# Optimization experiments

Measured on AMD Instinct MI355X. Metric: run time of the kernel, lower is better.

Reference implementation:

```python
import jax, jax.numpy as jnp
import numpy as np

B, T, C, H = 16, 4096, 256, 256

def setup_inputs() -> dict:
    key = jax.random.key(0)
    kx, kwi, kbi, kwh, kbh = jax.random.split(key, 5)
    s = 1.0 / np.sqrt(C)
    return {
        "x": jax.random.normal(kx, (B, T, C), dtype=jnp.float32),
        "Wi": jax.random.uniform(kwi, (H, C), dtype=jnp.float32, minval=-s, maxval=s),
        "bi": jax.random.uniform(kbi, (H,), dtype=jnp.float32, minval=-s, maxval=s),
        "Wh": jax.random.uniform(kwh, (H, H), dtype=jnp.float32, minval=-s, maxval=s),
        "bh": jax.random.uniform(kbh, (H,), dtype=jnp.float32, minval=-s, maxval=s),
    }

def reference(x, Wi, bi, Wh, bh):
    # Faithful to the source: Cell computes tanh(i2h(x) + h2h(x)) -- both
    # linears applied to x_t, the hidden state is never consumed, so there
    # is no recurrence and all timesteps can be computed in one fused pass.
    # hidden_states: [B, T, H]
    hidden_states = jnp.tanh(
        jnp.einsum("btc,hc->bth", x, Wi) + bi
        + jnp.einsum("btc,hc->bth", x, Wh) + bh
    )
    h_last = hidden_states[:, -1, :]  # h after the loop
    return (hidden_states, h_last)
```

## Files before the change

kernel.cpp:

```cpp
#include <hip/hip_runtime.h>
#include <hip/hip_bf16.h>


using short8 = __attribute__((ext_vector_type(8))) short;
using f32x4  = __attribute__((ext_vector_type(4))) float;

constexpr int Bn = 16, Tn = 4096, Cn = 256, Hn = 256;
constexpr int Mn = Bn * Tn;
constexpr int BM = 128, BK = 64;

__device__ inline unsigned pack2_bf16(float a, float b) {
  unsigned ua = __float_as_uint(a);
  unsigned ub = __float_as_uint(b);
  ua += 0x7fffu + ((ua >> 16) & 1u);
  ub += 0x7fffu + ((ub >> 16) & 1u);
  return (ua >> 16) | (ub & 0xffff0000u);
}

__global__ __launch_bounds__(256) void prep_kernel(
    const float* __restrict__ Wi, const float* __restrict__ bi,
    const float* __restrict__ Wh, const float* __restrict__ bh,
    unsigned short* __restrict__ Wc, float* __restrict__ bc) {
  int idx = blockIdx.x * 256 + threadIdx.x;
  float w = Wi[idx] + Wh[idx];
  unsigned u = __float_as_uint(w);
  u += 0x7fffu + ((u >> 16) & 1u);
  Wc[idx] = (unsigned short)(u >> 16);
  if (blockIdx.x == 0) bc[threadIdx.x] = bi[threadIdx.x] + bh[threadIdx.x];
}

__global__ __launch_bounds__(256, 2) void gemm_tanh_kernel(
    const float* __restrict__ x, const unsigned short* __restrict__ Wc,
    const float* __restrict__ bc, float* __restrict__ out) {
  __shared__ __align__(16) unsigned short Asm[BM * BK];
  __shared__ __align__(16) unsigned short Bsm[256 * BK];

  const int tid  = threadIdx.x;
  const int lane = tid & 63;
  const int wave = tid >> 6;
  const int wm   = wave >> 1;
  const int wn   = wave & 1;
  const int rid  = lane & 15;
  const int kgrp = lane >> 4;
  const int mBase = blockIdx.x * BM;

  f32x4 acc[4][8];
#pragma unroll
  for (int i = 0; i < 4; i++)
#pragma unroll
    for (int j = 0; j < 8; j++) acc[i][j] = (f32x4)0.f;

  for (int k0 = 0; k0 < Cn; k0 += BK) {
#pragma unroll
    for (int i = 0; i < 4; i++) {
      int h = i * 256 + tid;
      int r = h >> 3;
      int c = h & 7;
      const float4* src =
          (const float4*)(x + (size_t)(mBase + r) * Cn + k0) + c * 2;
      float4 v0 = src[0];
      float4 v1 = src[1];
      uint4 p;
      p.x = pack2_bf16(v0.x, v0.y);
      p.y = pack2_bf16(v0.z, v0.w);
      p.z = pack2_bf16(v1.x, v1.y);
      p.w = pack2_bf16(v1.z, v1.w);
      int pc = c ^ (r & 7);
      *(uint4*)&Asm[(r << 6) + (pc << 3)] = p;
    }
#pragma unroll
    for (int i = 0; i < 8; i++) {
      int h = i * 256 + tid;
      int r = h >> 3;
      int c = h & 7;
      uint4 v = *(const uint4*)(Wc + r * Cn + k0 + c * 8);
      int pc = c ^ (r & 7);
      *(uint4*)&Bsm[(r << 6) + (pc << 3)] = v;
    }
    __syncthreads();

#pragma unroll
    for (int khalf = 0; khalf < 2; khalf++) {
      const int chunk = (khalf << 2) | kgrp;
      short8 af[4], bf[8];
#pragma unroll
      for (int im = 0; im < 4; im++) {
        int row = wm * 64 + im * 16 + rid;
        af[im] = *(const short8*)&Asm[(row << 6) + ((chunk ^ (rid & 7)) << 3)];
      }
#pragma unroll
      for (int in = 0; in < 8; in++) {
        int row = wn * 128 + in * 16 + rid;
        bf[in] = *(const short8*)&Bsm[(row << 6) + ((chunk ^ (rid & 7)) << 3)];
      }
#pragma unroll
      for (int im = 0; im < 4; im++)
#pragma unroll
        for (int in = 0; in < 8; in++)
          acc[im][in] = __builtin_amdgcn_mfma_f32_16x16x32_bf16(
              af[im], bf[in], acc[im][in], 0, 0, 0);
    }
    __syncthreads();
  }

#pragma unroll
  for (int in = 0; in < 8; in++) {
    int n = wn * 128 + in * 16 + rid;
    float bias = bc[n];
#pragma unroll
    for (int im = 0; im < 4; im++) {
      int mrow = mBase + wm * 64 + im * 16 + kgrp * 4;
#pragma unroll
      for (int r = 0; r < 4; r++) {
        int m = mrow + r;
        float v = acc[im][in][r] + bias;
        float t = 1.f - 2.f / (__expf(2.f * v) + 1.f);
        out[(size_t)m * Hn + n] = t;
        if ((m & (Tn - 1)) == (Tn - 1))
          out[(size_t)Mn * Hn + (size_t)(m >> 12) * Hn + n] = t;
      }
    }
  }
}

extern "C" void kernel_launch(void* const* d_in, const int* in_sizes, int n_in,
                              void* d_out, int out_size, void* d_ws,
                              size_t ws_size, hipStream_t stream) {
  (void)in_sizes; (void)n_in; (void)out_size; (void)ws_size;
  const float* x  = (const float*)d_in[0];
  const float* Wi = (const float*)d_in[1];
  const float* bi = (const float*)d_in[2];
  const float* Wh = (const float*)d_in[3];
  const float* bh = (const float*)d_in[4];
  float* out = (float*)d_out;

  unsigned short* Wc = (unsigned short*)d_ws;
  float* bc = (float*)((char*)d_ws + (size_t)Hn * Cn * sizeof(unsigned short));

  prep_kernel<<<(Hn * Cn) / 256, 256, 0, stream>>>(Wi, bi, Wh, bh, Wc, bc);
  gemm_tanh_kernel<<<Mn / BM, 256, 0, stream>>>(x, Wc, bc, out);
}
```

Before: 132.9 us.

## Persistent kernel with register-resident weights and double-buffered x tiles

Replaces the 512-block tiled GEMM with 256 persistent blocks of 1024 threads. Each wave keeps its 16 output columns of the combined bf16 weight in registers for the whole K range, and the block loops over 32-row tiles of x. The next x tile is prefetched into registers and written to a second LDS buffer while MFMAs run on the current one. This drops the per-tile reload of the weight matrix through LDS and overlaps global loads with compute, but each wave now issues few MFMAs per tile and stores narrow 16-column output strips, so latency hiding and store coalescing may get worse.

```diff
diff --git a/kernel.cpp b/kernel.cpp
--- a/kernel.cpp
+++ b/kernel.cpp
@@ -1,13 +1,15 @@
 #include <hip/hip_runtime.h>
-#include <hip/hip_bf16.h>
 
 
 using short8 = __attribute__((ext_vector_type(8))) short;
 using f32x4  = __attribute__((ext_vector_type(4))) float;
 
 constexpr int Bn = 16, Tn = 4096, Cn = 256, Hn = 256;
-constexpr int Mn = Bn * Tn;
-constexpr int BM = 128, BK = 64;
+constexpr int Mn    = Bn * Tn;
+constexpr int BM    = 32;
+constexpr int NBLK  = 256;
+constexpr int TILES = Mn / BM;
+constexpr int ITERS = TILES / NBLK;
 
 __device__ inline unsigned pack2_bf16(float a, float b) {
   unsigned ua = __float_as_uint(a);
@@ -29,97 +31,95 @@
   if (blockIdx.x == 0) bc[threadIdx.x] = bi[threadIdx.x] + bh[threadIdx.x];
 }
 
-__global__ __launch_bounds__(256, 2) void gemm_tanh_kernel(
+__global__ __launch_bounds__(1024, 4) void gemm_tanh_kernel(
     const float* __restrict__ x, const unsigned short* __restrict__ Wc,
     const float* __restrict__ bc, float* __restrict__ out) {
-  __shared__ __align__(16) unsigned short Asm[BM * BK];
-  __shared__ __align__(16) unsigned short Bsm[256 * BK];
+  __shared__ __align__(16) unsigned short Asm[2][BM * Cn];
 
   const int tid  = threadIdx.x;
   const int lane = tid & 63;
   const int wave = tid >> 6;
-  const int wm   = wave >> 1;
-  const int wn   = wave & 1;
   const int rid  = lane & 15;
   const int kgrp = lane >> 4;
-  const int mBase = blockIdx.x * BM;
+  const int col  = wave * 16 + rid;
 
-  f32x4 acc[4][8];
+  short8 bf[8];
 #pragma unroll
-  for (int i = 0; i < 4; i++)
+  for (int ks = 0; ks < 8; ks++)
+    bf[ks] = *(const short8*)&Wc[col * Cn + ks * 32 + kgrp * 8];
+  const float bias = bc[col];
+
+  const int sr  = tid >> 5;
+  const int sc  = tid & 31;
+  const int swz = ((sc ^ (sr & 7)) << 3);
+
+  f32x4 acc[2];
+  acc[0] = (f32x4)0.f;
+  acc[1] = (f32x4)0.f;
+
+  float4 v0, v1;
+
+  {
+    const float4* src =
+        (const float4*)(x + (size_t)(blockIdx.x * BM + sr) * Cn + sc * 8);
+    v0 = src[0];
+    v1 = src[1];
+    uint4 p;
+    p.x = pack2_bf16(v0.x, v0.y);
+    p.y = pack2_bf16(v0.z, v0.w);
+    p.z = pack2_bf16(v1.x, v1.y);
+    p.w = pack2_bf16(v1.z, v1.w);
+    *(uint4*)&Asm[0][sr * Cn + swz] = p;
+  }
+  __syncthreads();
+
+  for (int t = 0; t < ITERS; t++) {
+    const int cur = t & 1;
+    const int m0  = (blockIdx.x + t * NBLK) * BM;
+
+    if (t + 1 < ITERS) {
+      const float4* src =
+          (const float4*)(x + (size_t)(m0 + NBLK * BM + sr) * Cn + sc * 8);
+      v0 = src[0];
+      v1 = src[1];
+    }
+
 #pragma unroll
-    for (int j = 0; j < 8; j++) acc[i][j] = (f32x4)0.f;
+    for (int ks = 0; ks < 8; ks++) {
+#pragma unroll
+      for (int mt = 0; mt < 2; mt++) {
+        int row = mt * 16 + rid;
+        short8 a = *(const short8*)
+            &Asm[cur][row * Cn + ((((ks << 2) | kgrp) ^ (rid & 7)) << 3)];
+        acc[mt] = __builtin_amdgcn_mfma_f32_16x16x32_bf16(a, bf[ks], acc[mt],
+                                                          0, 0, 0);
+      }
+    }
 
-  for (int k0 = 0; k0 < Cn; k0 += BK) {
-#pragma unroll
-    for (int i = 0; i < 4; i++) {
-      int h = i * 256 + tid;
-      int r = h >> 3;
-      int c = h & 7;
-      const float4* src =
-          (const float4*)(x + (size_t)(mBase + r) * Cn + k0) + c * 2;
-      float4 v0 = src[0];
-      float4 v1 = src[1];
+    if (t + 1 < ITERS) {
       uint4 p;
       p.x = pack2_bf16(v0.x, v0.y);
       p.y = pack2_bf16(v0.z, v0.w);
       p.z = pack2_bf16(v1.x, v1.y);
       p.w = pack2_bf16(v1.z, v1.w);
-      int pc = c ^ (r & 7);
-      *(uint4*)&Asm[(r << 6) + (pc << 3)] = p;
+      *(uint4*)&Asm[cur ^ 1][sr * Cn + swz] = p;
     }
-#pragma unroll
-    for (int i = 0; i < 8; i++) {
-      int h = i * 256 + tid;
-      int r = h >> 3;
-      int c = h & 7;
-      uint4 v = *(const uint4*)(Wc + r * Cn + k0 + c * 8);
-      int pc = c ^ (r & 7);
-      *(uint4*)&Bsm[(r << 6) + (pc << 3)] = v;
-    }
-    __syncthreads();
 
 #pragma unroll
-    for (int khalf = 0; khalf < 2; khalf++) {
-      const int chunk = (khalf << 2) | kgrp;
-      short8 af[4], bf[8];
-#pragma unroll
-      for (int im = 0; im < 4; im++) {
-        int row = wm * 64 + im * 16 + rid;
-        af[im] = *(const short8*)&Asm[(row << 6) + ((chunk ^ (rid & 7)) << 3)];
-      }
-#pragma unroll
-      for (int in = 0; in < 8; in++) {
-        int row = wn * 128 + in * 16 + rid;
-        bf[in] = *(const short8*)&Bsm[(row << 6) + ((chunk ^ (rid & 7)) << 3)];
-      }
-#pragma unroll
-      for (int im = 0; im < 4; im++)
-#pragma unroll
-        for (int in = 0; in < 8; in++)
-          acc[im][in] = __builtin_amdgcn_mfma_f32_16x16x32_bf16(
-              af[im], bf[in], acc[im][in], 0, 0, 0);
-    }
-    __syncthreads();
-  }
-
-#pragma unroll
-  for (int in = 0; in < 8; in++) {
-    int n = wn * 128 + in * 16 + rid;
-    float bias = bc[n];
-#pragma unroll
-    for (int im = 0; im < 4; im++) {
-      int mrow = mBase + wm * 64 + im * 16 + kgrp * 4;
+    for (int mt = 0; mt < 2; mt++) {
 #pragma unroll
       for (int r = 0; r < 4; r++) {
-        int m = mrow + r;
-        float v = acc[im][in][r] + bias;
-        float t = 1.f - 2.f / (__expf(2.f * v) + 1.f);
-        out[(size_t)m * Hn + n] = t;
+        int m   = m0 + mt * 16 + kgrp * 4 + r;
+        float v = acc[mt][r] + bias;
+        float tv = 1.f - 2.f / (__expf(2.f * v) + 1.f);
+        out[(size_t)m * Hn + col] = tv;
         if ((m & (Tn - 1)) == (Tn - 1))
-          out[(size_t)Mn * Hn + (size_t)(m >> 12) * Hn + n] = t;
+          out[(size_t)Mn * Hn + (size_t)(m >> 12) * Hn + col] = tv;
       }
+      acc[mt] = (f32x4)0.f;
     }
+
+    if (t + 1 < ITERS) __syncthreads();
   }
 }
 
@@ -138,5 +138,5 @@
   float* bc = (float*)((char*)d_ws + (size_t)Hn * Cn * sizeof(unsigned short));
 
   prep_kernel<<<(Hn * Cn) / 256, 256, 0, stream>>>(Wi, bi, Wh, bh, Wc, bc);
-  gemm_tanh_kernel<<<Mn / BM, 256, 0, stream>>>(x, Wc, bc, out);
+  gemm_tanh_kernel<<<NBLK, 1024, 0, stream>>>(x, Wc, bc, out);
 }
```

Result: no change. 133.3 us (+0.3%).
